# Performance work log

Measured on AMD Instinct MI355X. Metric: run time of the kernel, lower is better.

Reference implementation:

```python
import jax, jax.numpy as jnp
import numpy as np

B, NIN, D = 2048, 64, 128
N_LCB, N_FMB, RANK = 32, 32, 24
DIM_HIDDEN = 1024
N_OUT = N_LCB + N_FMB  # == NIN -> identity residual
MAX_VAL = 1.0
EPS_LN_FMB_MIN, EPS_LN_FMB_MAX = 1e-11, 1e7
KERAS_LN_EPS = 1e-3


def setup_inputs() -> dict:
    key = jax.random.key(0)
    ks = jax.random.split(key, 9)
    def w(k, shape, fan):
        return (jax.random.normal(k, shape, jnp.float32) / np.sqrt(fan)).astype(jnp.float32)
    return {
        "x": jax.random.normal(ks[0], (B, NIN, D), jnp.float32),
        "noise": jax.random.uniform(ks[1], (B, N_OUT, D), jnp.float32),
        "w_lcb": w(ks[2], (NIN, N_LCB), NIN),
        "w_rank": w(ks[3], (NIN, RANK), NIN),
        "w1": w(ks[4], (NIN * RANK, DIM_HIDDEN), NIN * RANK),
        "w2": w(ks[5], (DIM_HIDDEN, DIM_HIDDEN), DIM_HIDDEN),
        "w3": w(ks[6], (DIM_HIDDEN, N_FMB * D), DIM_HIDDEN),
        "gamma": jnp.ones((D,), jnp.float32),
        "beta": jnp.zeros((D,), jnp.float32),
    }


def _forward(x, noise, w_lcb, w_rank, w1, w2, w3, gamma, beta):
    # ---- LinearCompressBlock: Dense over feature (emb-count) axis ----
    lcb = jnp.einsum("bnd,nm->bmd", x, w_lcb)  # (B, N_LCB, D)

    # ---- FactorizationMachineBlock ----
    # rank_layer on transposed input: (B, D, NIN) @ (NIN, RANK)
    r = jnp.einsum("bnd,nr->bdr", x, w_rank)          # (B, D, RANK)
    fm = jnp.einsum("bnd,bdr->bnr", x, r)             # (B, NIN, RANK)
    fm = fm.reshape(fm.shape[0], NIN * RANK)
    # custom LayerNorm (no affine, clipped std)
    mu = jnp.mean(fm, axis=-1, keepdims=True)
    cen = fm - mu
    std = jnp.sqrt(jnp.mean(cen * cen, axis=-1, keepdims=True))
    std = jnp.clip(std, EPS_LN_FMB_MIN, EPS_LN_FMB_MAX)
    fm = cen / std
    # MLP: 2 hidden relu layers + linear out, dropout=0 / inference
    h = jax.nn.relu(fm @ w1)
    h = jax.nn.relu(h @ w2)
    fmb = (h @ w3).reshape(-1, N_FMB, D)              # (B, N_FMB, D)

    out = jnp.concatenate((fmb, lcb), axis=1)          # (B, N_OUT, D)
    residual = x                                        # NIN == N_OUT -> identity

    safe = jnp.clip(out, -MAX_VAL, MAX_VAL)
    a = jnp.abs(safe)
    c = lambda t: jnp.clip(t, -MAX_VAL, MAX_VAL)

    # conv term: reshape to (B, N, D//8, 8), 1x1 conv with all-ones (8->8)
    # filter == group-sum broadcast back over the 8 lanes
    g = safe.reshape(safe.shape[0], N_OUT, D // 8, 8)
    conv = jnp.broadcast_to(g.sum(-1, keepdims=True), g.shape).reshape(safe.shape)

    extra = (
        c(jnp.log(a + 1.0))
        + c(jax.lax.rsqrt(a + 1.0))
        + c(jax.nn.softmax(safe, axis=-1))
        + c(jnp.tanh(safe))
        + c(jnp.where(safe >= 0, safe, 0.2 * safe))          # leaky_relu alpha=0.2
        + c(jnp.exp(safe))
        + c(jax.nn.softplus(safe))
        + c(jnp.log1p(a))
        + jnp.zeros_like(safe)                               # zeros_like term
        + c(jnp.round(safe))
        + jnp.ones_like(safe)                                # pow(a+eps, 0) == 1
        + c(jnp.sign(safe))
        + c(jnp.prod(safe, axis=-1, keepdims=True))
        + c(jnp.isnan(safe).astype(jnp.float32))
        + c((~(safe < 0)).astype(jnp.float32))
        + c((safe != 0).astype(jnp.float32))
        + c((safe >= 0).astype(jnp.float32))
        + c(safe.astype(jnp.int8).astype(jnp.float32))       # bitwise_and(x,x)==x after int8 cast
        + c(jnp.max(safe, axis=-1, keepdims=True))
        + c(safe + safe)                                     # add_n([safe, safe])
        + c(safe + safe)                                     # raw Add
        + 7.0 * safe                                         # slice/split-concat/merge/einsum/squeeze/pad/stack identities (|safe|<=1 so clip no-op)
        + c(jnp.where(safe > 0.5, -1.0, safe))               # tensor_scatter_nd_update
        + c(conv)
        + c(noise)                                           # tf.random.uniform (deterministic input)
        + c(jnp.arange(D, dtype=jnp.float32))                # broadcast over last axis
        + c(jnp.sum(safe[0] * safe[0], axis=-1))[None, :, None]  # DiagPart(matmul(safe[0], safe[0]^T))
    )

    pre = out + residual + 1e-10 * extra
    # keras LayerNormalization(axis=-1), default epsilon=1e-3
    m = jnp.mean(pre, axis=-1, keepdims=True)
    v = jnp.mean(jnp.square(pre - m), axis=-1, keepdims=True)
    return (pre - m) * jax.lax.rsqrt(v + KERAS_LN_EPS) * gamma + beta


def reference(x, noise, w_lcb, w_rank, w1, w2, w3, gamma, beta):
    return _forward(x, noise, w_lcb, w_rank, w1, w2, w3, gamma, beta)
```

## Files before the change

### kernel.cpp

```cpp
#include <hip/hip_runtime.h>


typedef _Float16 half8_t __attribute__((ext_vector_type(8)));
typedef float floatx4 __attribute__((ext_vector_type(4)));

#define B_SZ 2048
#define NIN 64
#define D_SZ 128
#define RANK 24
#define FMK (NIN * RANK)
#define HID 1024
#define NFMB_D (32 * 128)

__global__ __launch_bounds__(256) void transpose_cast(
    const float* __restrict__ w, _Float16* __restrict__ wt, int K, int N) {
  __shared__ float tile[32][33];
  const int tk = blockIdx.x * 32;
  const int tn = blockIdx.y * 32;
  const int tx = threadIdx.x & 31;
  const int ty = threadIdx.x >> 5;
#pragma unroll
  for (int i = 0; i < 4; i++) {
    int k = ty + i * 8;
    tile[k][tx] = w[(size_t)(tk + k) * N + (tn + tx)];
  }
  __syncthreads();
#pragma unroll
  for (int i = 0; i < 4; i++) {
    int n = ty + i * 8;
    wt[(size_t)(tn + n) * K + (tk + tx)] = (_Float16)tile[tx][n];
  }
}

#define LDX 65
#define LDR 132
__global__ __launch_bounds__(256) void front_kernel(
    const float* __restrict__ x, const float* __restrict__ w_rank,
    _Float16* __restrict__ fmn) {
  __shared__ __align__(16) float xs_t[D_SZ * LDX];
  __shared__ __align__(16) float rs_t[RANK * LDR];
  __shared__ float redbuf[8];
  const int b = blockIdx.x, t = threadIdx.x;
  const int lane = t & 63;
  const int w = __builtin_amdgcn_readfirstlane(t >> 6);
  const float4* xb4 = (const float4*)(x + (size_t)b * (NIN * D_SZ));
#pragma unroll
  for (int i = 0; i < 8; i++) {
    int it = t + i * 256;
    int n = it >> 5;
    int d0 = (it & 31) * 4;
    float4 v = xb4[it];
    xs_t[(d0 + 0) * LDX + n] = v.x;
    xs_t[(d0 + 1) * LDX + n] = v.y;
    xs_t[(d0 + 2) * LDX + n] = v.z;
    xs_t[(d0 + 3) * LDX + n] = v.w;
  }
  __syncthreads();
  {
    float r0[6] = {0, 0, 0, 0, 0, 0}, r1[6] = {0, 0, 0, 0, 0, 0};
    const float* xp0 = xs_t + lane * LDX;
    const float* xp1 = xs_t + (lane + 64) * LDX;
    const float* wrp = w_rank + w * 6;
#pragma unroll 4
    for (int n = 0; n < NIN; n++) {
      float xv0 = xp0[n];
      float xv1 = xp1[n];
#pragma unroll
      for (int jj = 0; jj < 6; jj++) {
        float wv = wrp[n * RANK + jj];
        r0[jj] += xv0 * wv;
        r1[jj] += xv1 * wv;
      }
    }
#pragma unroll
    for (int jj = 0; jj < 6; jj++) {
      rs_t[(w * 6 + jj) * LDR + lane] = r0[jj];
      rs_t[(w * 6 + jj) * LDR + lane + 64] = r1[jj];
    }
  }
  __syncthreads();
  float facc[6] = {0, 0, 0, 0, 0, 0};
  {
    const int n = lane;
    const float4* rs4 = (const float4*)rs_t;
#pragma unroll 2
    for (int d4 = 0; d4 < 32; d4++) {
      float xv0 = xs_t[(d4 * 4 + 0) * LDX + n];
      float xv1 = xs_t[(d4 * 4 + 1) * LDX + n];
      float xv2 = xs_t[(d4 * 4 + 2) * LDX + n];
      float xv3 = xs_t[(d4 * 4 + 3) * LDX + n];
#pragma unroll
      for (int jj = 0; jj < 6; jj++) {
        float4 rv = rs4[(w * 6 + jj) * 33 + d4];
        facc[jj] += xv0 * rv.x + xv1 * rv.y + xv2 * rv.z + xv3 * rv.w;
      }
    }
  }
  float s = 0.f, s2 = 0.f;
#pragma unroll
  for (int jj = 0; jj < 6; jj++) {
    s += facc[jj];
    s2 += facc[jj] * facc[jj];
  }
#pragma unroll
  for (int off = 1; off < 64; off <<= 1) {
    s += __shfl_xor(s, off);
    s2 += __shfl_xor(s2, off);
  }
  if (lane == 0) {
    redbuf[w * 2] = s;
    redbuf[w * 2 + 1] = s2;
  }
  __syncthreads();
  s = redbuf[0] + redbuf[2] + redbuf[4] + redbuf[6];
  s2 = redbuf[1] + redbuf[3] + redbuf[5] + redbuf[7];
  const float mu = s * (1.f / FMK);
  float var = s2 * (1.f / FMK) - mu * mu;
  var = var > 0.f ? var : 0.f;
  float sd = sqrtf(var);
  sd = sd < 1e-11f ? 1e-11f : (sd > 1e7f ? 1e7f : sd);
  const float inv = 1.f / sd;
  _Float16* ob = fmn + (size_t)b * FMK + lane * RANK + w * 6;
#pragma unroll
  for (int jj = 0; jj < 6; jj++) ob[jj] = (_Float16)((facc[jj] - mu) * inv);
}

template <int MT, bool RELU>
__global__ __launch_bounds__(256, 2) void gemm_bt(
    const _Float16* __restrict__ A, const _Float16* __restrict__ Bt,
    _Float16* __restrict__ C, int M, int N, int K) {
  constexpr int LDT = 40;
  constexpr int MI = MT / 32;
  __shared__ __align__(16) _Float16 As[MT * LDT];
  __shared__ __align__(16) _Float16 Bs[128 * LDT];
  const int m0 = blockIdx.x * MT;
  const int n0 = blockIdx.y * 128;
  const int t = threadIdx.x;
  const int wave = t >> 6, lane = t & 63;
  const int wr = wave >> 1, wc = wave & 1;
  const int q = lane >> 4, ln = lane & 15;
  const int srow = t >> 2;
  const int skc = t & 3;
  const _Float16* gA0 = A + (size_t)(m0 + srow) * K + skc * 8;
  const _Float16* gA1 = gA0 + (size_t)64 * K;
  const _Float16* gB0 = Bt + (size_t)(n0 + srow) * K + skc * 8;
  const _Float16* gB1 = gB0 + (size_t)64 * K;
  const int ldsw = srow * LDT + skc * 8;

  floatx4 acc[MI][4] = {};

  uint4 ra0 = *(const uint4*)(gA0);
  uint4 ra1;
  if constexpr (MT == 128) ra1 = *(const uint4*)(gA1);
  uint4 rb0 = *(const uint4*)(gB0);
  uint4 rb1 = *(const uint4*)(gB1);

  for (int k0 = 0;;) {
    __syncthreads();
    *(uint4*)&As[ldsw] = ra0;
    if constexpr (MT == 128) *(uint4*)&As[64 * LDT + ldsw] = ra1;
    *(uint4*)&Bs[ldsw] = rb0;
    *(uint4*)&Bs[64 * LDT + ldsw] = rb1;
    __syncthreads();
    k0 += 32;
    if (k0 < K) {
      ra0 = *(const uint4*)(gA0 + k0);
      if constexpr (MT == 128) ra1 = *(const uint4*)(gA1 + k0);
      rb0 = *(const uint4*)(gB0 + k0);
      rb1 = *(const uint4*)(gB1 + k0);
    }
    half8_t af[MI], bf[4];
#pragma unroll
    for (int i = 0; i < MI; i++)
      af[i] = *(const half8_t*)&As[(wr * (MT / 2) + i * 16 + ln) * LDT + q * 8];
#pragma unroll
    for (int j = 0; j < 4; j++)
      bf[j] = *(const half8_t*)&Bs[(wc * 64 + j * 16 + ln) * LDT + q * 8];
#pragma unroll
    for (int i = 0; i < MI; i++)
#pragma unroll
      for (int j = 0; j < 4; j++)
        acc[i][j] =
            __builtin_amdgcn_mfma_f32_16x16x32_f16(af[i], bf[j], acc[i][j], 0, 0, 0);
    if (k0 >= K) break;
  }

#pragma unroll
  for (int i = 0; i < MI; i++) {
#pragma unroll
    for (int r = 0; r < 4; r++) {
      size_t row = (size_t)(m0 + wr * (MT / 2) + i * 16 + q * 4 + r);
      _Float16* crow = C + row * N + n0 + wc * 64 + ln;
#pragma unroll
      for (int j = 0; j < 4; j++) {
        float v = acc[i][j][r];
        if (RELU) v = v > 0.f ? v : 0.f;
        crow[j * 16] = (_Float16)v;
      }
    }
  }
}

__global__ __launch_bounds__(256) void epilogue_kernel(
    const float* __restrict__ x, const _Float16* __restrict__ fmb,
    const float* __restrict__ w_lcb, const float* __restrict__ gamma,
    const float* __restrict__ beta, float* __restrict__ out) {
  __shared__ __align__(16) float xs[NIN * D_SZ];
  __shared__ __align__(16) _Float16 pre[NIN * D_SZ];
  __shared__ float mrow[64], rrow[64];
  const int b = blockIdx.x, t = threadIdx.x;
  const float* xb = x + (size_t)b * (NIN * D_SZ);
  for (int i = t; i < NIN * D_SZ / 4; i += 256)
    ((float4*)xs)[i] = ((const float4*)xb)[i];
  __syncthreads();
  const half8_t* fb8 = (const half8_t*)(fmb + (size_t)b * NFMB_D);
#pragma unroll
  for (int ii = 0; ii < 2; ii++) {
    int g = t + ii * 256;
    half8_t p = fb8[g];
    half8_t o;
#pragma unroll
    for (int k = 0; k < 8; k++) o[k] = (_Float16)((float)p[k] + xs[g * 8 + k]);
    *(half8_t*)&pre[g * 8] = o;
  }
  {
    const int dd = t & 127;
    const int mg = __builtin_amdgcn_readfirstlane(t >> 7);
    float acc[16];
#pragma unroll
    for (int k = 0; k < 16; k++) acc[k] = 0.f;
    const float4* w4 = (const float4*)(w_lcb + mg * 16);
#pragma unroll 4
    for (int n = 0; n < NIN; n++) {
      float xv = xs[n * D_SZ + dd];
      float4 w0 = w4[n * 8 + 0];
      float4 w1 = w4[n * 8 + 1];
      float4 w2 = w4[n * 8 + 2];
      float4 w3 = w4[n * 8 + 3];
      acc[0] += xv * w0.x;  acc[1] += xv * w0.y;
      acc[2] += xv * w0.z;  acc[3] += xv * w0.w;
      acc[4] += xv * w1.x;  acc[5] += xv * w1.y;
      acc[6] += xv * w1.z;  acc[7] += xv * w1.w;
      acc[8] += xv * w2.x;  acc[9] += xv * w2.y;
      acc[10] += xv * w2.z; acc[11] += xv * w2.w;
      acc[12] += xv * w3.x; acc[13] += xv * w3.y;
      acc[14] += xv * w3.z; acc[15] += xv * w3.w;
    }
#pragma unroll
    for (int k = 0; k < 16; k++) {
      int c = 32 + mg * 16 + k;
      pre[c * D_SZ + dd] = (_Float16)(acc[k] + xs[c * D_SZ + dd]);
    }
  }
  __syncthreads();
  {
    const int c = t >> 2, qd = t & 3;
    float s = 0.f, s2 = 0.f;
    const _Float16* pr = pre + c * 128 + qd * 32;
    for (int k = 0; k < 32; k++) {
      float v = (float)pr[(k + t) & 31];
      s += v;
      s2 += v * v;
    }
    s += __shfl_xor(s, 1);
    s2 += __shfl_xor(s2, 1);
    s += __shfl_xor(s, 2);
    s2 += __shfl_xor(s2, 2);
    if (qd == 0) {
      float m = s * (1.f / 128.f);
      float var = s2 * (1.f / 128.f) - m * m;
      mrow[c] = m;
      rrow[c] = rsqrtf(var + 1e-3f);
    }
  }
  __syncthreads();
  float4* ob4 = (float4*)(out + (size_t)b * (NIN * D_SZ));
  const float4* g4 = (const float4*)gamma;
  const float4* be4 = (const float4*)beta;
#pragma unroll
  for (int ii = 0; ii < 4; ii++) {
    int i8 = t + ii * 256;
    int c = i8 >> 4;
    int d8 = i8 & 15;
    float m = mrow[c], rstd = rrow[c];
    half8_t p = *(const half8_t*)&pre[i8 * 8];
    float4 g0 = g4[d8 * 2], g1 = g4[d8 * 2 + 1];
    float4 b0 = be4[d8 * 2], b1 = be4[d8 * 2 + 1];
    float4 o0, o1;
    o0.x = ((float)p[0] - m) * rstd * g0.x + b0.x;
    o0.y = ((float)p[1] - m) * rstd * g0.y + b0.y;
    o0.z = ((float)p[2] - m) * rstd * g0.z + b0.z;
    o0.w = ((float)p[3] - m) * rstd * g0.w + b0.w;
    o1.x = ((float)p[4] - m) * rstd * g1.x + b1.x;
    o1.y = ((float)p[5] - m) * rstd * g1.y + b1.y;
    o1.z = ((float)p[6] - m) * rstd * g1.z + b1.z;
    o1.w = ((float)p[7] - m) * rstd * g1.w + b1.w;
    ob4[i8 * 2] = o0;
    ob4[i8 * 2 + 1] = o1;
  }
}

extern "C" void kernel_launch(void* const* d_in, const int* in_sizes, int n_in,
                              void* d_out, int out_size, void* d_ws,
                              size_t ws_size, hipStream_t stream) {
  const float* x = (const float*)d_in[0];
  const float* w_lcb = (const float*)d_in[2];
  const float* w_rank = (const float*)d_in[3];
  const float* w1 = (const float*)d_in[4];
  const float* w2 = (const float*)d_in[5];
  const float* w3 = (const float*)d_in[6];
  const float* gamma = (const float*)d_in[7];
  const float* beta = (const float*)d_in[8];
  float* out = (float*)d_out;

  char* ws = (char*)d_ws;
  _Float16* w1t = (_Float16*)ws; ws += (size_t)HID * FMK * 2;
  _Float16* w2t = (_Float16*)ws; ws += (size_t)HID * HID * 2;
  _Float16* w3t = (_Float16*)ws; ws += (size_t)NFMB_D * HID * 2;
  _Float16* fmn = (_Float16*)ws; ws += (size_t)B_SZ * FMK * 2;
  _Float16* h1  = (_Float16*)ws; ws += (size_t)B_SZ * HID * 2;
  _Float16* h2  = (_Float16*)ws; ws += (size_t)B_SZ * HID * 2;
  _Float16* fmb = (_Float16*)ws; ws += (size_t)B_SZ * NFMB_D * 2;

  transpose_cast<<<dim3(FMK / 32, HID / 32), 256, 0, stream>>>(w1, w1t, FMK, HID);
  transpose_cast<<<dim3(HID / 32, HID / 32), 256, 0, stream>>>(w2, w2t, HID, HID);
  transpose_cast<<<dim3(HID / 32, NFMB_D / 32), 256, 0, stream>>>(w3, w3t, HID, NFMB_D);
  front_kernel<<<B_SZ, 256, 0, stream>>>(x, w_rank, fmn);
  gemm_bt<64, true><<<dim3(B_SZ / 64, HID / 128), 256, 0, stream>>>(fmn, w1t, h1, B_SZ, HID, FMK);
  gemm_bt<64, true><<<dim3(B_SZ / 64, HID / 128), 256, 0, stream>>>(h1, w2t, h2, B_SZ, HID, HID);
  gemm_bt<128, false><<<dim3(B_SZ / 128, NFMB_D / 128), 256, 0, stream>>>(h2, w3t, fmb, B_SZ, NFMB_D, HID);
  epilogue_kernel<<<B_SZ, 256, 0, stream>>>(x, fmb, w_lcb, gamma, beta, out);
}
```

Before: 303.6 us.

## Move rank and LCB projections to MFMA in front kernel, slim epilogue

```diff
diff --git a/kernel.cpp b/kernel.cpp
--- a/kernel.cpp
+++ b/kernel.cpp
@@ -2,6 +2,7 @@
 
 
 typedef _Float16 half8_t __attribute__((ext_vector_type(8)));
+typedef _Float16 half4_t __attribute__((ext_vector_type(4)));
 typedef float floatx4 __attribute__((ext_vector_type(4)));
 
 #define B_SZ 2048
@@ -32,75 +33,133 @@
   }
 }
 
-#define LDX 65
-#define LDR 132
-__global__ __launch_bounds__(256) void front_kernel(
+#define STX 72
+#define STN 136
+__global__ __launch_bounds__(256, 2) void front_kernel(
     const float* __restrict__ x, const float* __restrict__ w_rank,
-    _Float16* __restrict__ fmn) {
-  __shared__ __align__(16) float xs_t[D_SZ * LDX];
-  __shared__ __align__(16) float rs_t[RANK * LDR];
-  __shared__ float redbuf[8];
+    const float* __restrict__ w_lcb, _Float16* __restrict__ fmn,
+    _Float16* __restrict__ lcb16) {
+  constexpr int XT_OFF = 0;
+  constexpr int X16_OFF = 18432;
+  constexpr int RT_OFF = X16_OFF + 17408;
+  constexpr int WRT_OFF = RT_OFF + 8704;
+  constexpr int WLT_OFF = WRT_OFF + 4608;
+  constexpr int RED_OFF = WLT_OFF + 4608;
+  __shared__ __align__(16) char smem[RED_OFF + 32];
+  _Float16* xT = (_Float16*)(smem + XT_OFF);
+  _Float16* x16 = (_Float16*)(smem + X16_OFF);
+  _Float16* rT = (_Float16*)(smem + RT_OFF);
+  _Float16* wrT = (_Float16*)(smem + WRT_OFF);
+  _Float16* wlT = (_Float16*)(smem + WLT_OFF);
+  float* redbuf = (float*)(smem + RED_OFF);
+  _Float16* lcb_s = (_Float16*)(smem + X16_OFF);
+  _Float16* fmn_s = (_Float16*)(smem + RT_OFF);
+
   const int b = blockIdx.x, t = threadIdx.x;
   const int lane = t & 63;
   const int w = __builtin_amdgcn_readfirstlane(t >> 6);
-  const float4* xb4 = (const float4*)(x + (size_t)b * (NIN * D_SZ));
-#pragma unroll
-  for (int i = 0; i < 8; i++) {
-    int it = t + i * 256;
-    int n = it >> 5;
-    int d0 = (it & 31) * 4;
-    float4 v = xb4[it];
-    xs_t[(d0 + 0) * LDX + n] = v.x;
-    xs_t[(d0 + 1) * LDX + n] = v.y;
-    xs_t[(d0 + 2) * LDX + n] = v.z;
-    xs_t[(d0 + 3) * LDX + n] = v.w;
-  }
-  __syncthreads();
-  {
-    float r0[6] = {0, 0, 0, 0, 0, 0}, r1[6] = {0, 0, 0, 0, 0, 0};
-    const float* xp0 = xs_t + lane * LDX;
-    const float* xp1 = xs_t + (lane + 64) * LDX;
-    const float* wrp = w_rank + w * 6;
-#pragma unroll 4
-    for (int n = 0; n < NIN; n++) {
-      float xv0 = xp0[n];
-      float xv1 = xp1[n];
-#pragma unroll
-      for (int jj = 0; jj < 6; jj++) {
-        float wv = wrp[n * RANK + jj];
-        r0[jj] += xv0 * wv;
-        r1[jj] += xv1 * wv;
+  const int q = lane >> 4, ln = lane & 15;
+
+  const float4* xg4 = (const float4*)(x + (size_t)b * (NIN * D_SZ));
+#pragma unroll
+  for (int hh = 0; hh < 2; hh++) {
+    int bb = t + hh * 256;
+    int n0 = (bb >> 5) * 4;
+    int bd = bb & 31;
+    int d0 = bd * 4;
+    float4 L0 = xg4[(n0 + 0) * 32 + bd];
+    float4 L1 = xg4[(n0 + 1) * 32 + bd];
+    float4 L2 = xg4[(n0 + 2) * 32 + bd];
+    float4 L3 = xg4[(n0 + 3) * 32 + bd];
+    *(half4_t*)&x16[(n0 + 0) * STN + d0] =
+        half4_t{(_Float16)L0.x, (_Float16)L0.y, (_Float16)L0.z, (_Float16)L0.w};
+    *(half4_t*)&x16[(n0 + 1) * STN + d0] =
+        half4_t{(_Float16)L1.x, (_Float16)L1.y, (_Float16)L1.z, (_Float16)L1.w};
+    *(half4_t*)&x16[(n0 + 2) * STN + d0] =
+        half4_t{(_Float16)L2.x, (_Float16)L2.y, (_Float16)L2.z, (_Float16)L2.w};
+    *(half4_t*)&x16[(n0 + 3) * STN + d0] =
+        half4_t{(_Float16)L3.x, (_Float16)L3.y, (_Float16)L3.z, (_Float16)L3.w};
+    *(half4_t*)&xT[(d0 + 0) * STX + n0] =
+        half4_t{(_Float16)L0.x, (_Float16)L1.x, (_Float16)L2.x, (_Float16)L3.x};
+    *(half4_t*)&xT[(d0 + 1) * STX + n0] =
+        half4_t{(_Float16)L0.y, (_Float16)L1.y, (_Float16)L2.y, (_Float16)L3.y};
+    *(half4_t*)&xT[(d0 + 2) * STX + n0] =
+        half4_t{(_Float16)L0.z, (_Float16)L1.z, (_Float16)L2.z, (_Float16)L3.z};
+    *(half4_t*)&xT[(d0 + 3) * STX + n0] =
+        half4_t{(_Float16)L0.w, (_Float16)L1.w, (_Float16)L2.w, (_Float16)L3.w};
+  }
+#pragma unroll
+  for (int k = 0; k < 6; k++) {
+    int i = t + k * 256;
+    int n = i / 24, j = i - n * 24;
+    wrT[j * STX + n] = (_Float16)w_rank[i];
+  }
+#pragma unroll
+  for (int k = 0; k < 2; k++) {
+    int i = t + k * 256;
+    wrT[(24 + (i >> 6)) * STX + (i & 63)] = (_Float16)0.f;
+  }
+#pragma unroll
+  for (int k = 0; k < 8; k++) {
+    int i = t + k * 256;
+    wlT[(i & 31) * STX + (i >> 5)] = (_Float16)w_lcb[i];
+  }
+  __syncthreads();
+
+  floatx4 r_acc[2][2] = {};
+  floatx4 l_acc[2][2] = {};
+#pragma unroll
+  for (int k = 0; k < 2; k++) {
+    half8_t bfrag[2], ar[2], al[2];
+#pragma unroll
+    for (int ni = 0; ni < 2; ni++)
+      bfrag[ni] =
+          *(const half8_t*)&xT[((2 * w + ni) * 16 + ln) * STX + k * 32 + q * 8];
+#pragma unroll
+    for (int mi = 0; mi < 2; mi++) {
+      ar[mi] = *(const half8_t*)&wrT[(mi * 16 + ln) * STX + k * 32 + q * 8];
+      al[mi] = *(const half8_t*)&wlT[(mi * 16 + ln) * STX + k * 32 + q * 8];
+    }
+#pragma unroll
+    for (int mi = 0; mi < 2; mi++)
+#pragma unroll
+      for (int ni = 0; ni < 2; ni++) {
+        r_acc[mi][ni] = __builtin_amdgcn_mfma_f32_16x16x32_f16(
+            ar[mi], bfrag[ni], r_acc[mi][ni], 0, 0, 0);
+        l_acc[mi][ni] = __builtin_amdgcn_mfma_f32_16x16x32_f16(
+            al[mi], bfrag[ni], l_acc[mi][ni], 0, 0, 0);
       }
-    }
-#pragma unroll
-    for (int jj = 0; jj < 6; jj++) {
-      rs_t[(w * 6 + jj) * LDR + lane] = r0[jj];
-      rs_t[(w * 6 + jj) * LDR + lane + 64] = r1[jj];
-    }
-  }
-  __syncthreads();
-  float facc[6] = {0, 0, 0, 0, 0, 0};
-  {
-    const int n = lane;
-    const float4* rs4 = (const float4*)rs_t;
-#pragma unroll 2
-    for (int d4 = 0; d4 < 32; d4++) {
-      float xv0 = xs_t[(d4 * 4 + 0) * LDX + n];
-      float xv1 = xs_t[(d4 * 4 + 1) * LDX + n];
-      float xv2 = xs_t[(d4 * 4 + 2) * LDX + n];
-      float xv3 = xs_t[(d4 * 4 + 3) * LDX + n];
-#pragma unroll
-      for (int jj = 0; jj < 6; jj++) {
-        float4 rv = rs4[(w * 6 + jj) * 33 + d4];
-        facc[jj] += xv0 * rv.x + xv1 * rv.y + xv2 * rv.z + xv3 * rv.w;
-      }
+  }
+#pragma unroll
+  for (int mi = 0; mi < 2; mi++)
+#pragma unroll
+    for (int ni = 0; ni < 2; ni++)
+#pragma unroll
+      for (int rr = 0; rr < 4; rr++)
+        rT[(mi * 16 + q * 4 + rr) * STN + (2 * w + ni) * 16 + ln] =
+            (_Float16)r_acc[mi][ni][rr];
+  __syncthreads();
+
+  floatx4 f_acc[2] = {};
+#pragma unroll
+  for (int k = 0; k < 4; k++) {
+    half8_t af = *(const half8_t*)&x16[(w * 16 + ln) * STN + k * 32 + q * 8];
+#pragma unroll
+    for (int nj = 0; nj < 2; nj++) {
+      half8_t bf = *(const half8_t*)&rT[(nj * 16 + ln) * STN + k * 32 + q * 8];
+      f_acc[nj] =
+          __builtin_amdgcn_mfma_f32_16x16x32_f16(af, bf, f_acc[nj], 0, 0, 0);
     }
   }
   float s = 0.f, s2 = 0.f;
 #pragma unroll
-  for (int jj = 0; jj < 6; jj++) {
-    s += facc[jj];
-    s2 += facc[jj] * facc[jj];
+  for (int rr = 0; rr < 4; rr++) {
+    float v = f_acc[0][rr];
+    s += v;
+    s2 += v * v;
+    float v1 = (ln < 8) ? f_acc[1][rr] : 0.f;
+    s += v1;
+    s2 += v1 * v1;
   }
 #pragma unroll
   for (int off = 1; off < 64; off <<= 1) {
@@ -120,9 +179,32 @@
   float sd = sqrtf(var);
   sd = sd < 1e-11f ? 1e-11f : (sd > 1e7f ? 1e7f : sd);
   const float inv = 1.f / sd;
-  _Float16* ob = fmn + (size_t)b * FMK + lane * RANK + w * 6;
-#pragma unroll
-  for (int jj = 0; jj < 6; jj++) ob[jj] = (_Float16)((facc[jj] - mu) * inv);
+
+#pragma unroll
+  for (int nj = 0; nj < 2; nj++) {
+    int j = nj * 16 + ln;
+    if (j < RANK) {
+#pragma unroll
+      for (int rr = 0; rr < 4; rr++)
+        fmn_s[(w * 16 + q * 4 + rr) * RANK + j] =
+            (_Float16)((f_acc[nj][rr] - mu) * inv);
+    }
+  }
+#pragma unroll
+  for (int mi = 0; mi < 2; mi++)
+#pragma unroll
+    for (int ni = 0; ni < 2; ni++)
+#pragma unroll
+      for (int rr = 0; rr < 4; rr++)
+        lcb_s[(mi * 16 + q * 4 + rr) * 128 + (2 * w + ni) * 16 + ln] =
+            (_Float16)l_acc[mi][ni][rr];
+  __syncthreads();
+  half8_t* fg = (half8_t*)(fmn + (size_t)b * FMK);
+  if (t < FMK / 8) fg[t] = ((const half8_t*)fmn_s)[t];
+  half8_t* lg = (half8_t*)(lcb16 + (size_t)b * NFMB_D);
+#pragma unroll
+  for (int i = 0; i < 2; i++)
+    lg[t + i * 256] = ((const half8_t*)lcb_s)[t + i * 256];
 }
 
 template <int MT, bool RELU>
@@ -203,54 +285,29 @@
 
 __global__ __launch_bounds__(256) void epilogue_kernel(
     const float* __restrict__ x, const _Float16* __restrict__ fmb,
-    const float* __restrict__ w_lcb, const float* __restrict__ gamma,
+    const _Float16* __restrict__ lcb16, const float* __restrict__ gamma,
     const float* __restrict__ beta, float* __restrict__ out) {
-  __shared__ __align__(16) float xs[NIN * D_SZ];
   __shared__ __align__(16) _Float16 pre[NIN * D_SZ];
   __shared__ float mrow[64], rrow[64];
   const int b = blockIdx.x, t = threadIdx.x;
-  const float* xb = x + (size_t)b * (NIN * D_SZ);
-  for (int i = t; i < NIN * D_SZ / 4; i += 256)
-    ((float4*)xs)[i] = ((const float4*)xb)[i];
-  __syncthreads();
+  const float4* xb4 = (const float4*)(x + (size_t)b * (NIN * D_SZ));
   const half8_t* fb8 = (const half8_t*)(fmb + (size_t)b * NFMB_D);
-#pragma unroll
-  for (int ii = 0; ii < 2; ii++) {
+  const half8_t* lb8 = (const half8_t*)(lcb16 + (size_t)b * NFMB_D);
+#pragma unroll
+  for (int ii = 0; ii < 4; ii++) {
     int g = t + ii * 256;
-    half8_t p = fb8[g];
+    half8_t p = (g < 512) ? fb8[g] : lb8[g - 512];
+    float4 xa = xb4[g * 2], xc = xb4[g * 2 + 1];
     half8_t o;
-#pragma unroll
-    for (int k = 0; k < 8; k++) o[k] = (_Float16)((float)p[k] + xs[g * 8 + k]);
+    o[0] = (_Float16)((float)p[0] + xa.x);
+    o[1] = (_Float16)((float)p[1] + xa.y);
+    o[2] = (_Float16)((float)p[2] + xa.z);
+    o[3] = (_Float16)((float)p[3] + xa.w);
+    o[4] = (_Float16)((float)p[4] + xc.x);
+    o[5] = (_Float16)((float)p[5] + xc.y);
+    o[6] = (_Float16)((float)p[6] + xc.z);
+    o[7] = (_Float16)((float)p[7] + xc.w);
     *(half8_t*)&pre[g * 8] = o;
-  }
-  {
-    const int dd = t & 127;
-    const int mg = __builtin_amdgcn_readfirstlane(t >> 7);
-    float acc[16];
-#pragma unroll
-    for (int k = 0; k < 16; k++) acc[k] = 0.f;
-    const float4* w4 = (const float4*)(w_lcb + mg * 16);
-#pragma unroll 4
-    for (int n = 0; n < NIN; n++) {
-      float xv = xs[n * D_SZ + dd];
-      float4 w0 = w4[n * 8 + 0];
-      float4 w1 = w4[n * 8 + 1];
-      float4 w2 = w4[n * 8 + 2];
-      float4 w3 = w4[n * 8 + 3];
-      acc[0] += xv * w0.x;  acc[1] += xv * w0.y;
-      acc[2] += xv * w0.z;  acc[3] += xv * w0.w;
-      acc[4] += xv * w1.x;  acc[5] += xv * w1.y;
-      acc[6] += xv * w1.z;  acc[7] += xv * w1.w;
-      acc[8] += xv * w2.x;  acc[9] += xv * w2.y;
-      acc[10] += xv * w2.z; acc[11] += xv * w2.w;
-      acc[12] += xv * w3.x; acc[13] += xv * w3.y;
-      acc[14] += xv * w3.z; acc[15] += xv * w3.w;
-    }
-#pragma unroll
-    for (int k = 0; k < 16; k++) {
-      int c = 32 + mg * 16 + k;
-      pre[c * D_SZ + dd] = (_Float16)(acc[k] + xs[c * D_SZ + dd]);
-    }
   }
   __syncthreads();
   {
@@ -319,15 +376,16 @@
   _Float16* w3t = (_Float16*)ws; ws += (size_t)NFMB_D * HID * 2;
   _Float16* fmn = (_Float16*)ws; ws += (size_t)B_SZ * FMK * 2;
   _Float16* h1  = (_Float16*)ws; ws += (size_t)B_SZ * HID * 2;
-  _Float16* h2  = (_Float16*)ws; ws += (size_t)B_SZ * HID * 2;
   _Float16* fmb = (_Float16*)ws; ws += (size_t)B_SZ * NFMB_D * 2;
+  _Float16* lcb16 = (_Float16*)ws; ws += (size_t)B_SZ * NFMB_D * 2;
+  _Float16* h2 = fmn;
 
   transpose_cast<<<dim3(FMK / 32, HID / 32), 256, 0, stream>>>(w1, w1t, FMK, HID);
   transpose_cast<<<dim3(HID / 32, HID / 32), 256, 0, stream>>>(w2, w2t, HID, HID);
   transpose_cast<<<dim3(HID / 32, NFMB_D / 32), 256, 0, stream>>>(w3, w3t, HID, NFMB_D);
-  front_kernel<<<B_SZ, 256, 0, stream>>>(x, w_rank, fmn);
+  front_kernel<<<B_SZ, 256, 0, stream>>>(x, w_rank, w_lcb, fmn, lcb16);
   gemm_bt<64, true><<<dim3(B_SZ / 64, HID / 128), 256, 0, stream>>>(fmn, w1t, h1, B_SZ, HID, FMK);
   gemm_bt<64, true><<<dim3(B_SZ / 64, HID / 128), 256, 0, stream>>>(h1, w2t, h2, B_SZ, HID, HID);
   gemm_bt<128, false><<<dim3(B_SZ / 128, NFMB_D / 128), 256, 0, stream>>>(h2, w3t, fmb, B_SZ, NFMB_D, HID);
-  epilogue_kernel<<<B_SZ, 256, 0, stream>>>(x, fmb, w_lcb, gamma, beta, out);
-}
+  epilogue_kernel<<<B_SZ, 256, 0, stream>>>(x, fmb, lcb16, gamma, beta, out);
+}
```

After: 277.4 us. -8.6%, faster.
